# Kernel optimization log

Measured on AMD Instinct MI355X. Metric: run time of the kernel, lower is better.

The kernel has to match this reference:

```python
import jax, jax.numpy as jnp
import numpy as np

EMBED = 512; HEADS = 16; WIN = 8; SHIFT = 4

def _rel_pos_index(Wh, Ww):
    # WindowMSA.double_step_seq + transpose-sum + flip(1)
    seq1 = np.arange(0, (2 * Ww - 1) * Wh, 2 * Ww - 1)
    seq2 = np.arange(0, Ww)
    coords = (seq1[:, None] + seq2[None, :]).reshape(1, -1)
    idx = coords + coords.T            # (Wh*Ww, Wh*Ww)
    return idx[:, ::-1].copy()

def _attn_mask(H_pad, W_pad, win, shift, nf):
    # static (trace-time) shifted-window mask, values in {0, -100}
    img = np.zeros((H_pad, W_pad))
    cnt = 0
    for h in (slice(0, -win), slice(-win, -shift), slice(-shift, None)):
        for w in (slice(0, -win), slice(-win, -shift), slice(-shift, None)):
            img[h, w] = cnt
            cnt += 1
    mw = img.reshape(H_pad // win, win, W_pad // win, win).transpose(0, 2, 1, 3).reshape(-1, win * win)
    am = mw[:, None, :] - mw[:, :, None]
    am = np.where(am != 0, -100.0, 0.0)
    return np.tile(am, (1, 1, nf))     # (nW, N, nf*N)

def setup_inputs():
    key = jax.random.key(0)
    ks = jax.random.split(key, 8)
    B, H, W, C, nf = 8, 128, 128, EMBED, 2
    s = 0.02
    return {
        'q': jax.random.normal(ks[0], (B, H * W, C), jnp.float32),
        'kv': jax.random.normal(ks[1], (B, nf, H * W, C), jnp.float32),
        'H': H, 'W': W,
        'rpb_table': jax.random.normal(ks[2], ((2 * WIN - 1) ** 2, HEADS), jnp.float32) * s,
        'Wq': jax.random.normal(ks[3], (C, C), jnp.float32) * s,
        'bq': jnp.zeros((C,), jnp.float32),
        'Wkv': jax.random.normal(ks[4], (C, 2 * C), jnp.float32) * s,
        'bkv': jnp.zeros((2 * C,), jnp.float32),
        'Wo': jax.random.normal(ks[5], (C, C), jnp.float32) * s,
        'bo': jnp.zeros((C,), jnp.float32),
    }

def reference(q, kv, H, W, rpb_table, Wq, bq, Wkv, bkv, Wo, bo):
    B, L, C = q.shape
    nf = kv.shape[1]
    win, shift, heads = WIN, SHIFT, HEADS
    hd = C // heads
    scale = hd ** -0.5
    pad_b = (-H) % win
    pad_r = (-W) % win
    x = q.reshape(B, H, W, C)
    kvx = kv.reshape(B * nf, H, W, C)
    x = jnp.pad(x, ((0, 0), (0, pad_b), (0, pad_r), (0, 0)))
    kvx = jnp.pad(kvx, ((0, 0), (0, pad_b), (0, pad_r), (0, 0)))
    Hp, Wp = H + pad_b, W + pad_r
    nh, nw = Hp // win, Wp // win
    if shift > 0:
        x = jnp.roll(x, (-shift, -shift), (1, 2))
        kvx = jnp.roll(kvx, (-shift, -shift), (1, 2))
        mask = jnp.asarray(_attn_mask(Hp, Wp, win, shift, nf), q.dtype)
    else:
        mask = None
    Nq = win * win
    Nk = nf * Nq
    # window partition: (B, Hp, Wp, C) -> (B*nh*nw, Nq, C)
    qw = x.reshape(B, nh, win, nw, win, C).transpose(0, 1, 3, 2, 4, 5).reshape(B * nh * nw, Nq, C)
    # kv: (B*nf, Hp, Wp, C) -> (B*nh*nw, nf*Nq, C)
    kvw = kvx.reshape(B, nf, nh, win, nw, win, C).transpose(0, 2, 4, 1, 3, 5, 6).reshape(B * nh * nw, Nk, C)
    Bw = qw.shape[0]
    qh = (qw @ Wq + bq).reshape(Bw, Nq, heads, hd).transpose(0, 2, 1, 3) * scale
    kvp = (kvw @ Wkv + bkv).reshape(Bw, Nk, 2, heads, hd).transpose(2, 0, 3, 1, 4)
    kh, vh = kvp[0], kvp[1]
    attn = jnp.einsum('bhqd,bhkd->bhqk', qh, kh)
    rpi = jnp.asarray(_rel_pos_index(win, win).reshape(-1))
    rpb = rpb_table[rpi].reshape(Nq, Nq, heads).transpose(2, 0, 1)  # (heads, Nq, Nq)
    attn = attn + jnp.tile(rpb, (1, 1, nf))[None]
    if mask is not None:
        nW = mask.shape[0]
        attn = (attn.reshape(Bw // nW, nW, heads, Nq, Nk) + mask[None, :, None]).reshape(Bw, heads, Nq, Nk)
    attn = jax.nn.softmax(attn, axis=-1)
    ow = jnp.einsum('bhqk,bhkd->bqhd', attn, vh).reshape(Bw, Nq, C)
    ow = ow @ Wo + bo
    # window reverse
    x = ow.reshape(B, nh, nw, win, win, C).transpose(0, 1, 3, 2, 4, 5).reshape(B, Hp, Wp, C)
    if shift > 0:
        x = jnp.roll(x, (shift, shift), (1, 2))
    x = x[:, :H, :W, :].reshape(B, H * W, C)
    return x
```

## Files before the change

kernel.cpp:

```cpp
#include <hip/hip_runtime.h>

typedef unsigned short ushort_t;
typedef short bf16x8 __attribute__((ext_vector_type(8)));
typedef float f32x4 __attribute__((ext_vector_type(4)));

#define MFMA16(a, b, c) __builtin_amdgcn_mfma_f32_16x16x32_bf16(a, b, c, 0, 0, 0)

static __device__ __forceinline__ float bf2f(ushort_t u) {
  union { unsigned int i; float f; } v;
  v.i = ((unsigned int)u) << 16;
  return v.f;
}
static __device__ __forceinline__ ushort_t f2bf(float f) {
  union { float f; unsigned int i; } v;
  v.f = f;
  unsigned int u = v.i;
  u = u + 0x7fffu + ((u >> 16) & 1u);
  return (ushort_t)(u >> 16);
}
static __device__ __forceinline__ unsigned int cvtpk(float lo, float hi) {
  unsigned int r;
  asm("v_cvt_pk_bf16_f32 %0, %1, %2" : "=v"(r) : "v"(lo), "v"(hi));
  return r;
}
static __device__ __forceinline__ void gload16(const void* g, void* l) {
  __builtin_amdgcn_global_load_lds((const __attribute__((address_space(1))) void*)g,
                                   (__attribute__((address_space(3))) void*)l,
                                   16, 0, 0);
}

__global__ void ws_sentinel(float* out, unsigned long long ws) {
  if (blockIdx.x == 0 && threadIdx.x == 0)
    out[0] = 1.0e6f * (1.0f + (float)(ws >> 23));
}

__global__ __launch_bounds__(256) void wtrans(const float* __restrict__ in,
                                              ushort_t* __restrict__ out,
                                              int R, int C) {
  int idx = blockIdx.x * 256 + threadIdx.x;
  if (idx < R * C) {
    int r = idx / C, c = idx - r * C;
    out[c * R + r] = f2bf(in[idx]);
  }
}

template <bool AF32, bool CF32>
__global__ __launch_bounds__(256, 2) void gemm_bt(const void* __restrict__ Av,
                                                  const ushort_t* __restrict__ Bt,
                                                  const float* __restrict__ bias,
                                                  void* __restrict__ Cv,
                                                  int N, int Nt) {
  constexpr int K = 512;
  __shared__ unsigned char As[AF32 ? 128 * 32 * 4 : 128 * 32 * 2];
  __shared__ unsigned char Bs[128 * 32 * 2];
  const int t = threadIdx.x;
  const int l = t & 63;
  const int w = t >> 6;
  const int w32 = w * 32;
  const int wr = w >> 1, wc = w & 1;
  const int lrow = l & 15;

  const int bid = blockIdx.x;
  const int xcd = bid & 7;
  const int slot = bid >> 3;
  const int mt = xcd + 8 * (slot / Nt);
  const int nt = slot % Nt;
  const long m0 = (long)mt * 128;
  const int n0 = nt * 128;

  const int arow = l >> 3;
  const int acol = ((16 * (l & 7)) ^ ((arow & 7) << 4)) >> 2;
  const int brow = l >> 2;
  const int bcol = ((16 * (l & 3)) ^ ((brow & 3) << 4)) >> 1;

  const f32x4 fz = {0.f, 0.f, 0.f, 0.f};
  f32x4 acc[4][4];
#pragma unroll
  for (int i = 0; i < 4; i++)
#pragma unroll
    for (int j = 0; j < 4; j++) acc[i][j] = fz;

  for (int kk = 0; kk < K; kk += 32) {
    __syncthreads();
    if constexpr (AF32) {
#pragma unroll
      for (int i = 0; i < 4; i++) {
        const float* gp = (const float*)Av + (m0 + w32 + i * 8 + arow) * (long)K + kk + acol;
        gload16(gp, &As[(w32 + i * 8) * 128]);
      }
    } else {
#pragma unroll
      for (int i = 0; i < 2; i++) {
        const ushort_t* gp = (const ushort_t*)Av + (m0 + w32 + i * 16 + brow) * (long)K + kk + bcol;
        gload16(gp, &As[(w32 + i * 16) * 64]);
      }
    }
#pragma unroll
    for (int i = 0; i < 2; i++) {
      const ushort_t* gp = Bt + (long)(n0 + w32 + i * 16 + brow) * K + kk + bcol;
      gload16(gp, &Bs[(w32 + i * 16) * 64]);
    }
    __syncthreads();

    bf16x8 af[4], bfr[4];
    if constexpr (AF32) {
#pragma unroll
      for (int mi = 0; mi < 4; mi++) {
        const int aR = wr * 64 + mi * 16 + lrow;
        const int s = (aR & 7) << 4;
        const int c0 = (l >> 4) * 32;
        f32x4 x = *(const f32x4*)&As[aR * 128 + (c0 ^ s)];
        f32x4 y = *(const f32x4*)&As[aR * 128 + ((c0 + 16) ^ s)];
        union { unsigned int u[4]; bf16x8 v; } r;
        r.u[0] = cvtpk(x[0], x[1]);
        r.u[1] = cvtpk(x[2], x[3]);
        r.u[2] = cvtpk(y[0], y[1]);
        r.u[3] = cvtpk(y[2], y[3]);
        af[mi] = r.v;
      }
    } else {
#pragma unroll
      for (int mi = 0; mi < 4; mi++) {
        const int aR = wr * 64 + mi * 16 + lrow;
        af[mi] = *(const bf16x8*)&As[aR * 64 + (((l >> 4) * 16) ^ ((aR & 3) << 4))];
      }
    }
#pragma unroll
    for (int ni = 0; ni < 4; ni++) {
      const int bR = wc * 64 + ni * 16 + lrow;
      bfr[ni] = *(const bf16x8*)&Bs[bR * 64 + (((l >> 4) * 16) ^ ((bR & 3) << 4))];
    }
#pragma unroll
    for (int mi = 0; mi < 4; mi++)
#pragma unroll
      for (int ni = 0; ni < 4; ni++)
        acc[mi][ni] = MFMA16(af[mi], bfr[ni], acc[mi][ni]);
  }

#pragma unroll
  for (int mi = 0; mi < 4; mi++) {
    const long row0 = m0 + wr * 64 + mi * 16 + (l >> 4) * 4;
#pragma unroll
    for (int ni = 0; ni < 4; ni++) {
      const int col = n0 + wc * 64 + ni * 16 + lrow;
      const float bv = bias[col];
#pragma unroll
      for (int r = 0; r < 4; r++) {
        const float val = acc[mi][ni][r] + bv;
        if constexpr (CF32)
          ((float*)Cv)[(row0 + r) * N + col] = val;
        else
          ((ushort_t*)Cv)[(row0 + r) * N + col] = f2bf(val);
      }
    }
  }
}

__global__ __launch_bounds__(256, 1) void attn_k(const ushort_t* __restrict__ Qp,
                                                 const ushort_t* __restrict__ KVp,
                                                 const float* __restrict__ rpbt,
                                                 ushort_t* __restrict__ Ao) {
  __shared__ ushort_t P[64 * 136];
  __shared__ __align__(16) unsigned char poolKV[32 * 136 * 2];
  __shared__ float Ltab[225];
  ushort_t* Ks = (ushort_t*)poolKV;
  ushort_t* Vt = (ushort_t*)poolKV;
  const int t = threadIdx.x;
  const int l = t & 63;
  const int w = t >> 6;
  const int wnd = blockIdx.x;
  const int h = blockIdx.y;
  const int b = wnd >> 8;
  const int wh = (wnd >> 4) & 15;
  const int ww = wnd & 15;

  const int lrow = l & 15;
  const int lq = l >> 4;
  const int lk = lq * 8;

  auto qrow = [&](int q) -> long {
    int i = q >> 3, j = q & 7;
    int ho = (wh * 8 + i + 4) & 127;
    int wo = (ww * 8 + j + 4) & 127;
    return (long)((b << 14) + (ho << 7) + wo);
  };
  auto kvrow = [&](int kp) -> long {
    int f = kp >> 6, m = kp & 63;
    int i = m >> 3, j = m & 7;
    int ho = (wh * 8 + i + 4) & 127;
    int wo = (ww * 8 + j + 4) & 127;
    return (long)(((b * 2 + f) << 14) + (ho << 7) + wo);
  };
  auto cnt_of = [&](int m) -> int {
    int hr = wh * 8 + (m >> 3), wr2 = ww * 8 + (m & 7);
    int rh = hr < 120 ? 0 : (hr < 124 ? 1 : 2);
    int rw = wr2 < 120 ? 0 : (wr2 < 124 ? 1 : 2);
    return rh * 3 + rw;
  };
  auto cvec = [](int m) -> int { return 15 * (m >> 3) + (m & 7); };

#pragma unroll
  for (int i = 0; i < 2; i++) {
    const int row = w * 32 + i * 16 + (l >> 2);
    const ushort_t* gp = KVp + kvrow(row) * 1024 + h * 32 + (l & 3) * 8;
    gload16(gp, Ks + (w * 32 + i * 16) * 32);
  }
  for (int i = t; i < 225; i += 256) Ltab[i] = rpbt[i * 16 + h];

  bf16x8 af = *(const bf16x8*)(Qp + qrow(w * 16 + lrow) * 512 + h * 32 + lk);

  __syncthreads();

  const f32x4 fz = {0.f, 0.f, 0.f, 0.f};
  f32x4 s[8];
#pragma unroll
  for (int ni = 0; ni < 8; ni++) s[ni] = fz;
#pragma unroll
  for (int ni = 0; ni < 8; ni++) {
    bf16x8 kf = *(const bf16x8*)&Ks[(ni * 16 + lrow) * 32 + lk];
    s[ni] = MFMA16(af, kf, s[ni]);
  }

  const float scale = 0.17677669529663687f;
#pragma unroll
  for (int r = 0; r < 4; r++) {
    const int q = w * 16 + lq * 4 + r;
    const int cq = cnt_of(q);
    const int cqv = cvec(q);
    float mx = -3.0e38f;
#pragma unroll
    for (int ni = 0; ni < 8; ni++) {
      const int k63 = (ni * 16 + lrow) & 63;
      float v = s[ni][r] * scale + Ltab[cqv + cvec(63 - k63)];
      if (cnt_of(k63) != cq) v -= 100.f;
      s[ni][r] = v;
      mx = fmaxf(mx, v);
    }
    mx = fmaxf(mx, __shfl_xor(mx, 1));
    mx = fmaxf(mx, __shfl_xor(mx, 2));
    mx = fmaxf(mx, __shfl_xor(mx, 4));
    mx = fmaxf(mx, __shfl_xor(mx, 8));
    float sum = 0.f;
#pragma unroll
    for (int ni = 0; ni < 8; ni++) {
      float p = __expf(s[ni][r] - mx);
      s[ni][r] = p;
      sum += p;
    }
    sum += __shfl_xor(sum, 1);
    sum += __shfl_xor(sum, 2);
    sum += __shfl_xor(sum, 4);
    sum += __shfl_xor(sum, 8);
    const float inv = 1.f / sum;
#pragma unroll
    for (int ni = 0; ni < 8; ni++)
      P[q * 136 + ni * 16 + lrow] = f2bf(s[ni][r] * inv);
  }

  __syncthreads();

  {
    const int kp = t & 127;
    const int dh = t >> 7;
    const ushort_t* src = KVp + kvrow(kp) * 1024 + 512 + h * 32 + dh * 16;
    bf16x8 v0 = *(const bf16x8*)(src);
    bf16x8 v1 = *(const bf16x8*)(src + 8);
#pragma unroll
    for (int d = 0; d < 8; d++) {
      Vt[(dh * 16 + d) * 136 + kp] = (ushort_t)v0[d];
      Vt[(dh * 16 + 8 + d) * 136 + kp] = (ushort_t)v1[d];
    }
  }
  __syncthreads();

  f32x4 o[2] = {fz, fz};
#pragma unroll
  for (int ks = 0; ks < 4; ks++) {
    bf16x8 pf = *(const bf16x8*)&P[(w * 16 + lrow) * 136 + ks * 32 + lk];
#pragma unroll
    for (int ni = 0; ni < 2; ni++) {
      bf16x8 vf = *(const bf16x8*)&Vt[(ni * 16 + lrow) * 136 + ks * 32 + lk];
      o[ni] = MFMA16(pf, vf, o[ni]);
    }
  }

#pragma unroll
  for (int ni = 0; ni < 2; ni++)
#pragma unroll
    for (int r = 0; r < 4; r++) {
      const int q = w * 16 + lq * 4 + r;
      Ao[qrow(q) * 512 + h * 32 + ni * 16 + lrow] = f2bf(o[ni][r]);
    }
}

extern "C" void kernel_launch(void* const* d_in, const int* in_sizes, int n_in,
                              void* d_out, int out_size, void* d_ws, size_t ws_size,
                              hipStream_t stream) {
  (void)in_sizes; (void)n_in; (void)out_size;
  const float* q    = (const float*)d_in[0];
  const float* kv   = (const float*)d_in[1];
  const float* rpbt = (const float*)d_in[4];
  const float* Wq   = (const float*)d_in[5];
  const float* bq   = (const float*)d_in[6];
  const float* Wkv  = (const float*)d_in[7];
  const float* bkv  = (const float*)d_in[8];
  const float* Wo   = (const float*)d_in[9];
  const float* bo   = (const float*)d_in[10];
  float* out = (float*)d_out;

  const size_t QB  = 16384ULL * 512;
  const size_t KVB = 32768ULL * 1024;
  const size_t per_b_bytes = (QB + QB + KVB) * 2;
  const size_t fixed_bytes = (512ULL*512 + 512ULL*1024 + 512ULL*512) * 2;
  const size_t needed1 = fixed_bytes + per_b_bytes;

  if (ws_size < needed1) {
    ws_sentinel<<<dim3(1), 64, 0, stream>>>(out, (unsigned long long)ws_size);
    return;
  }

  int nbc = 8;
  while (nbc > 1 && fixed_bytes + (size_t)nbc * per_b_bytes > ws_size) nbc >>= 1;

  char* ws = (char*)d_ws;
  ushort_t* WqT  = (ushort_t*)ws;
  ushort_t* WkvT = WqT + 512 * 512;
  ushort_t* WoT  = WkvT + 512 * 1024;
  ushort_t* Qp   = (ushort_t*)(ws + fixed_bytes);
  ushort_t* Ao   = Qp + (size_t)nbc * QB;
  ushort_t* KVp  = Ao + (size_t)nbc * QB;

  wtrans<<<dim3(1024), 256, 0, stream>>>(Wq, WqT, 512, 512);
  wtrans<<<dim3(2048), 256, 0, stream>>>(Wkv, WkvT, 512, 1024);
  wtrans<<<dim3(1024), 256, 0, stream>>>(Wo, WoT, 512, 512);

  for (int c = 0; c < 8 / nbc; ++c) {
    const size_t b0 = (size_t)c * nbc;
    const int MtQ = nbc * 128;
    const int MtKV = nbc * 256;
    gemm_bt<true, false><<<dim3(MtQ * 4), 256, 0, stream>>>(q + b0 * QB, WqT, bq,
                                                            Qp, 512, 4);
    gemm_bt<true, false><<<dim3(MtKV * 8), 256, 0, stream>>>(kv + b0 * KVB / 2, WkvT,
                                                             bkv, KVp, 1024, 8);
    attn_k<<<dim3(nbc * 256, 16), 256, 0, stream>>>(Qp, KVp, rpbt, Ao);
    gemm_bt<false, true><<<dim3(MtQ * 4), 256, 0, stream>>>(Ao, WoT, bo,
                                                            out + b0 * QB, 512, 4);
  }
}
```

Baseline: 1.020 ms.

## Widen GEMM tiles to 128x256 with 8 waves and fuse weight transposes

The GEMM block grows from 256 to 512 threads (8 waves), and each block now covers a 128x256 output tile instead of 128x128. Each A tile, which for the projections is fp32 converted to bf16 in LDS, is therefore loaded once per 256 output columns, halving A re-reads. The three weight-transpose launches are merged into one kernel to cut launch overhead. In exchange, B shared memory doubles, which may limit occupancy, and the grid has half as many blocks.

```diff
diff --git a/kernel.cpp b/kernel.cpp
--- a/kernel.cpp
+++ b/kernel.cpp
@@ -34,31 +34,42 @@
     out[0] = 1.0e6f * (1.0f + (float)(ws >> 23));
 }
 
-__global__ __launch_bounds__(256) void wtrans(const float* __restrict__ in,
-                                              ushort_t* __restrict__ out,
-                                              int R, int C) {
+__global__ __launch_bounds__(256) void wtrans3(const float* __restrict__ Wq,
+                                               const float* __restrict__ Wkv,
+                                               const float* __restrict__ Wo,
+                                               ushort_t* __restrict__ WqT,
+                                               ushort_t* __restrict__ WkvT,
+                                               ushort_t* __restrict__ WoT) {
   int idx = blockIdx.x * 256 + threadIdx.x;
-  if (idx < R * C) {
-    int r = idx / C, c = idx - r * C;
-    out[c * R + r] = f2bf(in[idx]);
+  if (idx < 262144) {
+    int r = idx >> 9, c = idx & 511;
+    WqT[c * 512 + r] = f2bf(Wq[idx]);
+  } else if (idx < 786432) {
+    int i = idx - 262144;
+    int r = i >> 10, c = i & 1023;
+    WkvT[c * 512 + r] = f2bf(Wkv[i]);
+  } else if (idx < 1048576) {
+    int i = idx - 786432;
+    int r = i >> 9, c = i & 511;
+    WoT[c * 512 + r] = f2bf(Wo[i]);
   }
 }
 
 template <bool AF32, bool CF32>
-__global__ __launch_bounds__(256, 2) void gemm_bt(const void* __restrict__ Av,
+__global__ __launch_bounds__(512, 2) void gemm_bt(const void* __restrict__ Av,
                                                   const ushort_t* __restrict__ Bt,
                                                   const float* __restrict__ bias,
                                                   void* __restrict__ Cv,
                                                   int N, int Nt) {
   constexpr int K = 512;
-  __shared__ unsigned char As[AF32 ? 128 * 32 * 4 : 128 * 32 * 2];
-  __shared__ unsigned char Bs[128 * 32 * 2];
+  __shared__ __align__(16) unsigned char As[AF32 ? 128 * 32 * 4 : 128 * 32 * 2];
+  __shared__ __align__(16) unsigned char Bs[256 * 32 * 2];
   const int t = threadIdx.x;
   const int l = t & 63;
   const int w = t >> 6;
-  const int w32 = w * 32;
-  const int wr = w >> 1, wc = w & 1;
+  const int wr = w >> 2, wc = w & 3;
   const int lrow = l & 15;
+  const int g = l >> 4;
 
   const int bid = blockIdx.x;
   const int xcd = bid & 7;
@@ -66,7 +77,7 @@
   const int mt = xcd + 8 * (slot / Nt);
   const int nt = slot % Nt;
   const long m0 = (long)mt * 128;
-  const int n0 = nt * 128;
+  const int n0 = nt * 256;
 
   const int arow = l >> 3;
   const int acol = ((16 * (l & 7)) ^ ((arow & 7) << 4)) >> 2;
@@ -84,21 +95,18 @@
     __syncthreads();
     if constexpr (AF32) {
 #pragma unroll
-      for (int i = 0; i < 4; i++) {
-        const float* gp = (const float*)Av + (m0 + w32 + i * 8 + arow) * (long)K + kk + acol;
-        gload16(gp, &As[(w32 + i * 8) * 128]);
+      for (int i = 0; i < 2; i++) {
+        const float* gp = (const float*)Av + (m0 + w * 16 + i * 8 + arow) * (long)K + kk + acol;
+        gload16(gp, &As[(w * 16 + i * 8) * 128]);
       }
     } else {
-#pragma unroll
-      for (int i = 0; i < 2; i++) {
-        const ushort_t* gp = (const ushort_t*)Av + (m0 + w32 + i * 16 + brow) * (long)K + kk + bcol;
-        gload16(gp, &As[(w32 + i * 16) * 64]);
-      }
+      const ushort_t* gp = (const ushort_t*)Av + (m0 + w * 16 + brow) * (long)K + kk + bcol;
+      gload16(gp, &As[(w * 16) * 64]);
     }
 #pragma unroll
     for (int i = 0; i < 2; i++) {
-      const ushort_t* gp = Bt + (long)(n0 + w32 + i * 16 + brow) * K + kk + bcol;
-      gload16(gp, &Bs[(w32 + i * 16) * 64]);
+      const ushort_t* gp = Bt + (long)(n0 + w * 32 + i * 16 + brow) * K + kk + bcol;
+      gload16(gp, &Bs[(w * 32 + i * 16) * 64]);
     }
     __syncthreads();
 
@@ -108,7 +116,7 @@
       for (int mi = 0; mi < 4; mi++) {
         const int aR = wr * 64 + mi * 16 + lrow;
         const int s = (aR & 7) << 4;
-        const int c0 = (l >> 4) * 32;
+        const int c0 = g * 32;
         f32x4 x = *(const f32x4*)&As[aR * 128 + (c0 ^ s)];
         f32x4 y = *(const f32x4*)&As[aR * 128 + ((c0 + 16) ^ s)];
         union { unsigned int u[4]; bf16x8 v; } r;
@@ -122,13 +130,13 @@
 #pragma unroll
       for (int mi = 0; mi < 4; mi++) {
         const int aR = wr * 64 + mi * 16 + lrow;
-        af[mi] = *(const bf16x8*)&As[aR * 64 + (((l >> 4) * 16) ^ ((aR & 3) << 4))];
+        af[mi] = *(const bf16x8*)&As[aR * 64 + ((g * 16) ^ ((aR & 3) << 4))];
       }
     }
 #pragma unroll
     for (int ni = 0; ni < 4; ni++) {
       const int bR = wc * 64 + ni * 16 + lrow;
-      bfr[ni] = *(const bf16x8*)&Bs[bR * 64 + (((l >> 4) * 16) ^ ((bR & 3) << 4))];
+      bfr[ni] = *(const bf16x8*)&Bs[bR * 64 + ((g * 16) ^ ((bR & 3) << 4))];
     }
 #pragma unroll
     for (int mi = 0; mi < 4; mi++)
@@ -330,20 +338,18 @@
   ushort_t* Ao   = Qp + (size_t)nbc * QB;
   ushort_t* KVp  = Ao + (size_t)nbc * QB;
 
-  wtrans<<<dim3(1024), 256, 0, stream>>>(Wq, WqT, 512, 512);
-  wtrans<<<dim3(2048), 256, 0, stream>>>(Wkv, WkvT, 512, 1024);
-  wtrans<<<dim3(1024), 256, 0, stream>>>(Wo, WoT, 512, 512);
+  wtrans3<<<dim3(4096), 256, 0, stream>>>(Wq, Wkv, Wo, WqT, WkvT, WoT);
 
   for (int c = 0; c < 8 / nbc; ++c) {
     const size_t b0 = (size_t)c * nbc;
     const int MtQ = nbc * 128;
     const int MtKV = nbc * 256;
-    gemm_bt<true, false><<<dim3(MtQ * 4), 256, 0, stream>>>(q + b0 * QB, WqT, bq,
-                                                            Qp, 512, 4);
-    gemm_bt<true, false><<<dim3(MtKV * 8), 256, 0, stream>>>(kv + b0 * KVB / 2, WkvT,
-                                                             bkv, KVp, 1024, 8);
+    gemm_bt<true, false><<<dim3(MtQ * 2), 512, 0, stream>>>(q + b0 * QB, WqT, bq,
+                                                            Qp, 512, 2);
+    gemm_bt<true, false><<<dim3(MtKV * 4), 512, 0, stream>>>(kv + b0 * KVB / 2, WkvT,
+                                                             bkv, KVp, 1024, 4);
     attn_k<<<dim3(nbc * 256, 16), 256, 0, stream>>>(Qp, KVp, rpbt, Ao);
-    gemm_bt<false, true><<<dim3(MtQ * 4), 256, 0, stream>>>(Ao, WoT, bo,
-                                                            out + b0 * QB, 512, 4);
-  }
-}
+    gemm_bt<false, true><<<dim3(MtQ * 2), 512, 0, stream>>>(Ao, WoT, bo,
+                                                            out + b0 * QB, 512, 2);
+  }
+}
```

Measured after the change: 1.054 ms. 3.3% more time.
